# Optimization experiments

Measured on AMD Instinct MI355X. Metric: run time of the kernel, lower is better.

## Reference

```python
import jax, jax.numpy as jnp
import numpy as np

N_NODES = 2048


def setup_inputs() -> dict:
    key = jax.random.key(0)
    ks = jax.random.split(key, 10)
    s = 0.05
    return {
        "x": jax.random.normal(ks[0], (N_NODES, 32), dtype=jnp.float32),
        "centroids": jax.random.normal(ks[1], (N_NODES, 3), dtype=jnp.float32),
        "W_self1": jax.random.normal(ks[2], (35, 64), dtype=jnp.float32) * s,
        "W_neigh1": jax.random.normal(ks[3], (35, 64), dtype=jnp.float32) * s,
        "b1": jnp.zeros((64,), dtype=jnp.float32),
        "W_self2": jax.random.normal(ks[4], (64, 32), dtype=jnp.float32) * s,
        "W_neigh2": jax.random.normal(ks[5], (64, 32), dtype=jnp.float32) * s,
        "b2": jnp.zeros((32,), dtype=jnp.float32),
        "Wm1": jax.random.normal(ks[6], (64, 32), dtype=jnp.float32) * s,
        "bm1": jnp.zeros((32,), dtype=jnp.float32),
        "Wm2": jax.random.normal(ks[7], (32, 2), dtype=jnp.float32) * s,
        "bm2": jnp.zeros((2,), dtype=jnp.float32),
    }


def reference(x, centroids, W_self1, W_neigh1, b1, W_self2, W_neigh2, b2,
              Wm1, bm1, Wm2, bm2):
    n = x.shape[0]
    # Complete DAG edge list: edges i -> j for all i < j (static indices).
    src, dst = jnp.triu_indices(n, k=1)  # each [E], E = n(n-1)/2

    # --- edge features: per-feature cosine-sim vector + |centroid diff| ---
    norms = jnp.linalg.norm(x, axis=1)                       # [N]
    cos = (x[src] * x[dst]) / (norms[src] * norms[dst])[:, None]   # [E,32]
    cdiff = jnp.abs(centroids[src] - centroids[dst])               # [E,3]
    edge_weight = jnp.concatenate([cos, cdiff], axis=1)            # [E,35]

    h = jnp.concatenate([x, centroids], axis=1)                    # [N,35]

    # in-degree of each destination node (mean aggregator denominator)
    deg = jnp.zeros((n,), dtype=h.dtype).at[dst].add(1.0)
    inv_deg = jnp.where(deg > 0, 1.0 / jnp.maximum(deg, 1.0), 0.0)[:, None]

    # --- SAGEConv 1 (mean, with per-feature edge weights) ---
    msg1 = h[src] * edge_weight                                    # [E,35]
    neigh1 = jax.ops.segment_sum(msg1, dst, num_segments=n) * inv_deg
    h1 = h @ W_self1 + neigh1 @ W_neigh1 + b1                      # [N,64]

    # --- SAGEConv 2 (mean, no edge weight) ---
    neigh2 = jax.ops.segment_sum(h1[src], dst, num_segments=n) * inv_deg
    h2 = h1 @ W_self2 + neigh2 @ W_neigh2 + b2                     # [N,32]

    # --- pairwise edge gather + MLP head ---
    ef = jnp.concatenate([h2[src], h2[dst]], axis=1)               # [E,64]
    hid = jax.nn.relu(ef @ Wm1 + bm1)                              # [E,32]
    out = jax.nn.softmax(hid @ Wm2 + bm2, axis=-1)                 # [E,2]
    return out
```

## Files before the change

### kernel.cpp

```cpp
#include <hip/hip_runtime.h>
#include <math.h>

#define N_NODES 2048
#define N1S 36

__device__ __forceinline__ float invdeg(int j) { return j > 0 ? 1.0f / (float)j : 0.0f; }

__global__ __launch_bounds__(256) void k_edgefeat(const float* __restrict__ x,
                                                  const float* __restrict__ cent,
                                                  float* __restrict__ n1) {
  const int tid = threadIdx.x;
  const int bx = blockIdx.x;
  if (bx < 32) {
    __shared__ float invn_s[N_NODES];
    __shared__ float sc[256];
    const int f = bx;
    for (int r = 0; r < 8; ++r) {
      int n = tid + 256 * r;
      const float4* xp = (const float4*)(x + n * 32);
      float s = 0.f;
#pragma unroll
      for (int q = 0; q < 8; ++q) {
        float4 v = xp[q];
        s += v.x * v.x + v.y * v.y + v.z * v.z + v.w * v.w;
      }
      invn_s[n] = rsqrtf(s);
    }
    __syncthreads();
    float sv[8], xv[8];
    float ts = 0.f;
#pragma unroll
    for (int r = 0; r < 8; ++r) {
      int i = tid * 8 + r;
      float xf = x[i * 32 + f];
      xv[r] = xf;
      float s = xf * xf * invn_s[i];
      sv[r] = s;
      ts += s;
    }
    sc[tid] = ts;
    __syncthreads();
    for (int off = 1; off < 256; off <<= 1) {
      float v = (tid >= off) ? sc[tid - off] : 0.f;
      __syncthreads();
      sc[tid] += v;
      __syncthreads();
    }
    float P = sc[tid] - ts;
#pragma unroll
    for (int r = 0; r < 8; ++r) {
      int i = tid * 8 + r;
      n1[i * N1S + f] = P * xv[r] * invn_s[i] * invdeg(i);
      P += sv[r];
    }
  } else {
    __shared__ float cs[N_NODES * 3];
    const float4* cp = (const float4*)cent;
    float4* csp = (float4*)cs;
#pragma unroll
    for (int q = 0; q < 6; ++q) csp[tid + 256 * q] = cp[tid + 256 * q];
    __syncthreads();
    const int w = (bx - 32) * 4 + (tid >> 6);
    const int lane = tid & 63;
#pragma unroll
    for (int pick = 0; pick < 2; ++pick) {
      const int j = pick ? (2047 - w) : w;
      const float cj0 = cs[j * 3 + 0], cj1 = cs[j * 3 + 1], cj2 = cs[j * 3 + 2];
      float s0 = 0.f, s1 = 0.f, s2 = 0.f;
      for (int i = lane; i < j; i += 64) {
        float c0 = cs[i * 3 + 0], c1 = cs[i * 3 + 1], c2 = cs[i * 3 + 2];
        s0 += c0 * fabsf(c0 - cj0);
        s1 += c1 * fabsf(c1 - cj1);
        s2 += c2 * fabsf(c2 - cj2);
      }
#pragma unroll
      for (int d = 32; d > 0; d >>= 1) {
        s0 += __shfl_down(s0, d);
        s1 += __shfl_down(s1, d);
        s2 += __shfl_down(s2, d);
      }
      if (lane == 0) {
        float idg = invdeg(j);
        n1[j * N1S + 32] = s0 * idg;
        n1[j * N1S + 33] = s1 * idg;
        n1[j * N1S + 34] = s2 * idg;
      }
    }
  }
}

__global__ __launch_bounds__(256) void k_h1(const float* __restrict__ x,
                                            const float* __restrict__ cent,
                                            const float* __restrict__ n1,
                                            const float* __restrict__ Ws1,
                                            const float* __restrict__ Wn1,
                                            const float* __restrict__ b1,
                                            float* __restrict__ h1,
                                            float* __restrict__ h1T) {
  const int tid = threadIdx.x;
  const int n = __builtin_amdgcn_readfirstlane(blockIdx.x * 4 + (tid >> 6));
  const int o = tid & 63;
  float acc = b1[o];
  const float4* xr = (const float4*)(x + n * 32);
  const float4* nr = (const float4*)(n1 + n * N1S);
#pragma unroll
  for (int q = 0; q < 8; ++q) {
    float4 xv = xr[q];
    float4 nv = nr[q];
    acc += xv.x * Ws1[(4 * q + 0) * 64 + o] + nv.x * Wn1[(4 * q + 0) * 64 + o];
    acc += xv.y * Ws1[(4 * q + 1) * 64 + o] + nv.y * Wn1[(4 * q + 1) * 64 + o];
    acc += xv.z * Ws1[(4 * q + 2) * 64 + o] + nv.z * Wn1[(4 * q + 2) * 64 + o];
    acc += xv.w * Ws1[(4 * q + 3) * 64 + o] + nv.w * Wn1[(4 * q + 3) * 64 + o];
  }
  {
    float4 nv = nr[8];
    float c0 = cent[n * 3 + 0], c1 = cent[n * 3 + 1], c2 = cent[n * 3 + 2];
    acc += c0 * Ws1[32 * 64 + o] + nv.x * Wn1[32 * 64 + o];
    acc += c1 * Ws1[33 * 64 + o] + nv.y * Wn1[33 * 64 + o];
    acc += c2 * Ws1[34 * 64 + o] + nv.z * Wn1[34 * 64 + o];
  }
  h1[n * 64 + o] = acc;
  h1T[o * N_NODES + n] = acc;
}

__global__ __launch_bounds__(256) void k_scan_h1(const float* __restrict__ h1T,
                                                 float* __restrict__ n2) {
  __shared__ float sc[256];
  const int tid = threadIdx.x;
  const int o = blockIdx.x;
  float sv[8];
  const float4* colp = (const float4*)(h1T + o * N_NODES);
  float4 a = colp[2 * tid];
  float4 b = colp[2 * tid + 1];
  sv[0] = a.x; sv[1] = a.y; sv[2] = a.z; sv[3] = a.w;
  sv[4] = b.x; sv[5] = b.y; sv[6] = b.z; sv[7] = b.w;
  float ts = 0.f;
#pragma unroll
  for (int r = 0; r < 8; ++r) ts += sv[r];
  sc[tid] = ts;
  __syncthreads();
  for (int off = 1; off < 256; off <<= 1) {
    float v = (tid >= off) ? sc[tid - off] : 0.f;
    __syncthreads();
    sc[tid] += v;
    __syncthreads();
  }
  float P = sc[tid] - ts;
#pragma unroll
  for (int r = 0; r < 8; ++r) {
    int i = tid * 8 + r;
    n2[i * 64 + o] = P * invdeg(i);
    P += sv[r];
  }
}

__global__ __launch_bounds__(256) void k_h2AB(const float* __restrict__ h1,
                                              const float* __restrict__ n2,
                                              const float* __restrict__ Ws2,
                                              const float* __restrict__ Wn2,
                                              const float* __restrict__ b2,
                                              const float* __restrict__ Wm1,
                                              const float* __restrict__ bm1,
                                              float* __restrict__ A,
                                              float* __restrict__ Bm) {
  __shared__ float h2s[4][32];
  const int tid = threadIdx.x;
  const int wv = tid >> 6;
  const int lane = tid & 63;
  const int o = lane & 31;
  const int half = lane >> 5;
  const int n = __builtin_amdgcn_readfirstlane(blockIdx.x * 4 + wv);
  float acc = b2[o];
#pragma unroll
  for (int f = 0; f < 64; ++f)
    acc += h1[n * 64 + f] * Ws2[f * 32 + o] + n2[n * 64 + f] * Wn2[f * 32 + o];
  h2s[wv][o] = acc;
  __syncthreads();
  float r = half ? bm1[o] : 0.f;
#pragma unroll
  for (int f = 0; f < 32; ++f)
    r += h2s[wv][f] * Wm1[(half * 32 + f) * 32 + o];
  if (half)
    Bm[n * 32 + o] = r;
  else
    A[n * 32 + o] = r;
}

__global__ __launch_bounds__(256) void k_edges(const float* __restrict__ A,
                                               const float* __restrict__ Bm,
                                               const float* __restrict__ Wm2,
                                               const float* __restrict__ bm2,
                                               float2* __restrict__ out) {
  const int tid = threadIdx.x;
  const int j0 = blockIdx.x * 256;
  const int i0 = blockIdx.y * 8;
  if (i0 >= j0 + 255) return;
  const int j = j0 + tid;
  float Br[32];
  const float4* bp = (const float4*)(Bm + j * 32);
#pragma unroll
  for (int q = 0; q < 8; ++q) {
    float4 v = bp[q];
    Br[4 * q + 0] = v.x;
    Br[4 * q + 1] = v.y;
    Br[4 * q + 2] = v.z;
    Br[4 * q + 3] = v.w;
  }
  float wd[32];
#pragma unroll
  for (int f = 0; f < 32; ++f)
    wd[f] = Wm2[f * 2 + 1] - Wm2[f * 2];
  const float db = bm2[1] - bm2[0];
#pragma unroll
  for (int ii = 0; ii < 8; ++ii) {
    const int i = i0 + ii;
    const float* Ar = A + i * 32;
    float d = db;
#pragma unroll
    for (int f = 0; f < 32; ++f)
      d += fmaxf(Ar[f] + Br[f], 0.f) * wd[f];
    if (i < j) {
      float p0 = 1.0f / (1.0f + __expf(d));
      int e = i * (2 * N_NODES - 1 - i) / 2 + (j - i - 1);
      out[e] = make_float2(p0, 1.0f - p0);
    }
  }
}

extern "C" void kernel_launch(void* const* d_in, const int* in_sizes, int n_in,
                              void* d_out, int out_size, void* d_ws, size_t ws_size,
                              hipStream_t stream) {
  const float* x    = (const float*)d_in[0];
  const float* cent = (const float*)d_in[1];
  const float* Ws1  = (const float*)d_in[2];
  const float* Wn1  = (const float*)d_in[3];
  const float* b1   = (const float*)d_in[4];
  const float* Ws2  = (const float*)d_in[5];
  const float* Wn2  = (const float*)d_in[6];
  const float* b2   = (const float*)d_in[7];
  const float* Wm1  = (const float*)d_in[8];
  const float* bm1  = (const float*)d_in[9];
  const float* Wm2  = (const float*)d_in[10];
  const float* bm2  = (const float*)d_in[11];

  float* ws  = (float*)d_ws;
  float* n1  = ws;
  float* h1  = n1 + 2048 * N1S;
  float* h1T = h1 + 2048 * 64;
  float* n2  = h1T + 2048 * 64;
  float* A   = n2 + 2048 * 64;
  float* Bm  = A + 2048 * 32;

  k_edgefeat<<<288, 256, 0, stream>>>(x, cent, n1);
  k_h1<<<512, 256, 0, stream>>>(x, cent, n1, Ws1, Wn1, b1, h1, h1T);
  k_scan_h1<<<64, 256, 0, stream>>>(h1T, n2);
  k_h2AB<<<512, 256, 0, stream>>>(h1, n2, Ws2, Wn2, b2, Wm1, bm1, A, Bm);
  k_edges<<<dim3(8, 256), 256, 0, stream>>>(A, Bm, Wm2, bm2, (float2*)d_out);
}
```

Measured before the change: 120.8 us.

## Fuse all five stages into one cooperative kernel with grid syncs

```diff
diff --git a/kernel.cpp b/kernel.cpp
--- a/kernel.cpp
+++ b/kernel.cpp
@@ -1,19 +1,33 @@
 #include <hip/hip_runtime.h>
+#include <hip/hip_cooperative_groups.h>
 #include <math.h>
+
+namespace cg = cooperative_groups;
 
 #define N_NODES 2048
 #define N1S 36
+#define NBLK 512
 
 __device__ __forceinline__ float invdeg(int j) { return j > 0 ? 1.0f / (float)j : 0.0f; }
 
-__global__ __launch_bounds__(256) void k_edgefeat(const float* __restrict__ x,
-                                                  const float* __restrict__ cent,
-                                                  float* __restrict__ n1) {
+__global__ __launch_bounds__(256, 2) void k_fused(
+    const float* __restrict__ x, const float* __restrict__ cent,
+    const float* __restrict__ Ws1, const float* __restrict__ Wn1,
+    const float* __restrict__ b1, const float* __restrict__ Ws2,
+    const float* __restrict__ Wn2, const float* __restrict__ b2,
+    const float* __restrict__ Wm1, const float* __restrict__ bm1,
+    const float* __restrict__ Wm2, const float* __restrict__ bm2,
+    float* __restrict__ n1, float* __restrict__ h1, float* __restrict__ h1T,
+    float* __restrict__ n2, float* __restrict__ A, float* __restrict__ Bm,
+    float2* __restrict__ out) {
+  cg::grid_group grid = cg::this_grid();
+  __shared__ float smem[6144];
   const int tid = threadIdx.x;
   const int bx = blockIdx.x;
+
   if (bx < 32) {
-    __shared__ float invn_s[N_NODES];
-    __shared__ float sc[256];
+    float* invn_s = smem;
+    float* sc = smem + 2048;
     const int f = bx;
     for (int r = 0; r < 8; ++r) {
       int n = tid + 256 * r;
@@ -53,8 +67,8 @@
       n1[i * N1S + f] = P * xv[r] * invn_s[i] * invdeg(i);
       P += sv[r];
     }
-  } else {
-    __shared__ float cs[N_NODES * 3];
+  } else if (bx < 288) {
+    float* cs = smem;
     const float4* cp = (const float4*)cent;
     float4* csp = (float4*)cs;
 #pragma unroll
@@ -87,142 +101,127 @@
       }
     }
   }
-}
-
-__global__ __launch_bounds__(256) void k_h1(const float* __restrict__ x,
-                                            const float* __restrict__ cent,
-                                            const float* __restrict__ n1,
-                                            const float* __restrict__ Ws1,
-                                            const float* __restrict__ Wn1,
-                                            const float* __restrict__ b1,
-                                            float* __restrict__ h1,
-                                            float* __restrict__ h1T) {
-  const int tid = threadIdx.x;
-  const int n = __builtin_amdgcn_readfirstlane(blockIdx.x * 4 + (tid >> 6));
-  const int o = tid & 63;
-  float acc = b1[o];
-  const float4* xr = (const float4*)(x + n * 32);
-  const float4* nr = (const float4*)(n1 + n * N1S);
-#pragma unroll
-  for (int q = 0; q < 8; ++q) {
-    float4 xv = xr[q];
-    float4 nv = nr[q];
-    acc += xv.x * Ws1[(4 * q + 0) * 64 + o] + nv.x * Wn1[(4 * q + 0) * 64 + o];
-    acc += xv.y * Ws1[(4 * q + 1) * 64 + o] + nv.y * Wn1[(4 * q + 1) * 64 + o];
-    acc += xv.z * Ws1[(4 * q + 2) * 64 + o] + nv.z * Wn1[(4 * q + 2) * 64 + o];
-    acc += xv.w * Ws1[(4 * q + 3) * 64 + o] + nv.w * Wn1[(4 * q + 3) * 64 + o];
-  }
+  grid.sync();
+
   {
-    float4 nv = nr[8];
-    float c0 = cent[n * 3 + 0], c1 = cent[n * 3 + 1], c2 = cent[n * 3 + 2];
-    acc += c0 * Ws1[32 * 64 + o] + nv.x * Wn1[32 * 64 + o];
-    acc += c1 * Ws1[33 * 64 + o] + nv.y * Wn1[33 * 64 + o];
-    acc += c2 * Ws1[34 * 64 + o] + nv.z * Wn1[34 * 64 + o];
-  }
-  h1[n * 64 + o] = acc;
-  h1T[o * N_NODES + n] = acc;
-}
-
-__global__ __launch_bounds__(256) void k_scan_h1(const float* __restrict__ h1T,
-                                                 float* __restrict__ n2) {
-  __shared__ float sc[256];
-  const int tid = threadIdx.x;
-  const int o = blockIdx.x;
-  float sv[8];
-  const float4* colp = (const float4*)(h1T + o * N_NODES);
-  float4 a = colp[2 * tid];
-  float4 b = colp[2 * tid + 1];
-  sv[0] = a.x; sv[1] = a.y; sv[2] = a.z; sv[3] = a.w;
-  sv[4] = b.x; sv[5] = b.y; sv[6] = b.z; sv[7] = b.w;
-  float ts = 0.f;
-#pragma unroll
-  for (int r = 0; r < 8; ++r) ts += sv[r];
-  sc[tid] = ts;
-  __syncthreads();
-  for (int off = 1; off < 256; off <<= 1) {
-    float v = (tid >= off) ? sc[tid - off] : 0.f;
-    __syncthreads();
-    sc[tid] += v;
-    __syncthreads();
-  }
-  float P = sc[tid] - ts;
-#pragma unroll
-  for (int r = 0; r < 8; ++r) {
-    int i = tid * 8 + r;
-    n2[i * 64 + o] = P * invdeg(i);
-    P += sv[r];
-  }
-}
-
-__global__ __launch_bounds__(256) void k_h2AB(const float* __restrict__ h1,
-                                              const float* __restrict__ n2,
-                                              const float* __restrict__ Ws2,
-                                              const float* __restrict__ Wn2,
-                                              const float* __restrict__ b2,
-                                              const float* __restrict__ Wm1,
-                                              const float* __restrict__ bm1,
-                                              float* __restrict__ A,
-                                              float* __restrict__ Bm) {
-  __shared__ float h2s[4][32];
-  const int tid = threadIdx.x;
-  const int wv = tid >> 6;
-  const int lane = tid & 63;
-  const int o = lane & 31;
-  const int half = lane >> 5;
-  const int n = __builtin_amdgcn_readfirstlane(blockIdx.x * 4 + wv);
-  float acc = b2[o];
-#pragma unroll
-  for (int f = 0; f < 64; ++f)
-    acc += h1[n * 64 + f] * Ws2[f * 32 + o] + n2[n * 64 + f] * Wn2[f * 32 + o];
-  h2s[wv][o] = acc;
-  __syncthreads();
-  float r = half ? bm1[o] : 0.f;
-#pragma unroll
-  for (int f = 0; f < 32; ++f)
-    r += h2s[wv][f] * Wm1[(half * 32 + f) * 32 + o];
-  if (half)
-    Bm[n * 32 + o] = r;
-  else
-    A[n * 32 + o] = r;
-}
-
-__global__ __launch_bounds__(256) void k_edges(const float* __restrict__ A,
-                                               const float* __restrict__ Bm,
-                                               const float* __restrict__ Wm2,
-                                               const float* __restrict__ bm2,
-                                               float2* __restrict__ out) {
-  const int tid = threadIdx.x;
-  const int j0 = blockIdx.x * 256;
-  const int i0 = blockIdx.y * 8;
-  if (i0 >= j0 + 255) return;
-  const int j = j0 + tid;
-  float Br[32];
-  const float4* bp = (const float4*)(Bm + j * 32);
-#pragma unroll
-  for (int q = 0; q < 8; ++q) {
-    float4 v = bp[q];
-    Br[4 * q + 0] = v.x;
-    Br[4 * q + 1] = v.y;
-    Br[4 * q + 2] = v.z;
-    Br[4 * q + 3] = v.w;
-  }
-  float wd[32];
-#pragma unroll
-  for (int f = 0; f < 32; ++f)
-    wd[f] = Wm2[f * 2 + 1] - Wm2[f * 2];
-  const float db = bm2[1] - bm2[0];
-#pragma unroll
-  for (int ii = 0; ii < 8; ++ii) {
-    const int i = i0 + ii;
-    const float* Ar = A + i * 32;
-    float d = db;
+    const int n = __builtin_amdgcn_readfirstlane(bx * 4 + (tid >> 6));
+    const int o = tid & 63;
+    float acc = b1[o];
+    const float4* xr = (const float4*)(x + n * 32);
+    const float4* nr = (const float4*)(n1 + n * N1S);
+#pragma unroll
+    for (int q = 0; q < 8; ++q) {
+      float4 xv = xr[q];
+      float4 nv = nr[q];
+      acc += xv.x * Ws1[(4 * q + 0) * 64 + o] + nv.x * Wn1[(4 * q + 0) * 64 + o];
+      acc += xv.y * Ws1[(4 * q + 1) * 64 + o] + nv.y * Wn1[(4 * q + 1) * 64 + o];
+      acc += xv.z * Ws1[(4 * q + 2) * 64 + o] + nv.z * Wn1[(4 * q + 2) * 64 + o];
+      acc += xv.w * Ws1[(4 * q + 3) * 64 + o] + nv.w * Wn1[(4 * q + 3) * 64 + o];
+    }
+    {
+      float4 nv = nr[8];
+      float c0 = cent[n * 3 + 0], c1 = cent[n * 3 + 1], c2 = cent[n * 3 + 2];
+      acc += c0 * Ws1[32 * 64 + o] + nv.x * Wn1[32 * 64 + o];
+      acc += c1 * Ws1[33 * 64 + o] + nv.y * Wn1[33 * 64 + o];
+      acc += c2 * Ws1[34 * 64 + o] + nv.z * Wn1[34 * 64 + o];
+    }
+    h1[n * 64 + o] = acc;
+    h1T[o * N_NODES + n] = acc;
+  }
+  grid.sync();
+
+  if (bx < 64) {
+    float* sc = smem;
+    const int o = bx;
+    float sv[8];
+    const float4* colp = (const float4*)(h1T + o * N_NODES);
+    float4 a = colp[2 * tid];
+    float4 b = colp[2 * tid + 1];
+    sv[0] = a.x; sv[1] = a.y; sv[2] = a.z; sv[3] = a.w;
+    sv[4] = b.x; sv[5] = b.y; sv[6] = b.z; sv[7] = b.w;
+    float ts = 0.f;
+#pragma unroll
+    for (int r = 0; r < 8; ++r) ts += sv[r];
+    sc[tid] = ts;
+    __syncthreads();
+    for (int off = 1; off < 256; off <<= 1) {
+      float v = (tid >= off) ? sc[tid - off] : 0.f;
+      __syncthreads();
+      sc[tid] += v;
+      __syncthreads();
+    }
+    float P = sc[tid] - ts;
+#pragma unroll
+    for (int r = 0; r < 8; ++r) {
+      int i = tid * 8 + r;
+      n2[i * 64 + o] = P * invdeg(i);
+      P += sv[r];
+    }
+  }
+  grid.sync();
+
+  {
+    float* h2s = smem;
+    const int wv = tid >> 6;
+    const int lane = tid & 63;
+    const int o = lane & 31;
+    const int half = lane >> 5;
+    const int n = __builtin_amdgcn_readfirstlane(bx * 4 + wv);
+    float acc = b2[o];
+#pragma unroll
+    for (int f = 0; f < 64; ++f)
+      acc += h1[n * 64 + f] * Ws2[f * 32 + o] + n2[n * 64 + f] * Wn2[f * 32 + o];
+    h2s[wv * 32 + o] = acc;
+    __syncthreads();
+    float r = half ? bm1[o] : 0.f;
 #pragma unroll
     for (int f = 0; f < 32; ++f)
-      d += fmaxf(Ar[f] + Br[f], 0.f) * wd[f];
-    if (i < j) {
-      float p0 = 1.0f / (1.0f + __expf(d));
-      int e = i * (2 * N_NODES - 1 - i) / 2 + (j - i - 1);
-      out[e] = make_float2(p0, 1.0f - p0);
+      r += h2s[wv * 32 + f] * Wm1[(half * 32 + f) * 32 + o];
+    if (half)
+      Bm[n * 32 + o] = r;
+    else
+      A[n * 32 + o] = r;
+  }
+  grid.sync();
+
+  {
+    float wd[32];
+#pragma unroll
+    for (int f = 0; f < 32; ++f)
+      wd[f] = Wm2[f * 2 + 1] - Wm2[f * 2];
+    const float db = bm2[1] - bm2[0];
+    for (int s = bx; s < 1152; s += NBLK) {
+      int bxe = 0;
+#pragma unroll
+      for (int k = 1; k < 8; ++k) bxe += (s >= 16 * k * (k + 1)) ? 1 : 0;
+      const int bye = s - 16 * bxe * (bxe + 1);
+      const int j0 = bxe * 256;
+      const int i0 = bye * 8;
+      const int j = j0 + tid;
+      float Br[32];
+      const float4* bp = (const float4*)(Bm + j * 32);
+#pragma unroll
+      for (int q = 0; q < 8; ++q) {
+        float4 v = bp[q];
+        Br[4 * q + 0] = v.x;
+        Br[4 * q + 1] = v.y;
+        Br[4 * q + 2] = v.z;
+        Br[4 * q + 3] = v.w;
+      }
+#pragma unroll
+      for (int ii = 0; ii < 8; ++ii) {
+        const int i = i0 + ii;
+        const float* Ar = A + i * 32;
+        float d = db;
+#pragma unroll
+        for (int f = 0; f < 32; ++f)
+          d += fmaxf(Ar[f] + Br[f], 0.f) * wd[f];
+        if (i < j) {
+          float p0 = 1.0f / (1.0f + __expf(d));
+          int e = i * (2 * N_NODES - 1 - i) / 2 + (j - i - 1);
+          out[e] = make_float2(p0, 1.0f - p0);
+        }
+      }
     }
   }
 }
@@ -250,10 +249,10 @@
   float* n2  = h1T + 2048 * 64;
   float* A   = n2 + 2048 * 64;
   float* Bm  = A + 2048 * 32;
-
-  k_edgefeat<<<288, 256, 0, stream>>>(x, cent, n1);
-  k_h1<<<512, 256, 0, stream>>>(x, cent, n1, Ws1, Wn1, b1, h1, h1T);
-  k_scan_h1<<<64, 256, 0, stream>>>(h1T, n2);
-  k_h2AB<<<512, 256, 0, stream>>>(h1, n2, Ws2, Wn2, b2, Wm1, bm1, A, Bm);
-  k_edges<<<dim3(8, 256), 256, 0, stream>>>(A, Bm, Wm2, bm2, (float2*)d_out);
+  float2* outp = (float2*)d_out;
+
+  void* args[] = {&x, &cent, &Ws1, &Wn1, &b1, &Ws2, &Wn2, &b2,
+                  &Wm1, &bm1, &Wm2, &bm2,
+                  &n1, &h1, &h1T, &n2, &A, &Bm, &outp};
+  hipLaunchCooperativeKernel((void*)k_fused, dim3(NBLK), dim3(256), args, 0, stream);
 }
```

Measured after the change: 342.4 us. 183% more time.

## Fuse h1 prefix-sum scan into neighbouring kernels and compact triangular edge grid

Applied to the files above, without the earlier changes.

```diff
diff --git a/kernel.cpp b/kernel.cpp
--- a/kernel.cpp
+++ b/kernel.cpp
@@ -96,9 +96,11 @@
                                             const float* __restrict__ Wn1,
                                             const float* __restrict__ b1,
                                             float* __restrict__ h1,
-                                            float* __restrict__ h1T) {
-  const int tid = threadIdx.x;
-  const int n = __builtin_amdgcn_readfirstlane(blockIdx.x * 4 + (tid >> 6));
+                                            float* __restrict__ csum) {
+  __shared__ float h1s[4][64];
+  const int tid = threadIdx.x;
+  const int wv = tid >> 6;
+  const int n = __builtin_amdgcn_readfirstlane(blockIdx.x * 4 + wv);
   const int o = tid & 63;
   float acc = b1[o];
   const float4* xr = (const float4*)(x + n * 32);
@@ -120,42 +122,15 @@
     acc += c2 * Ws1[34 * 64 + o] + nv.z * Wn1[34 * 64 + o];
   }
   h1[n * 64 + o] = acc;
-  h1T[o * N_NODES + n] = acc;
-}
-
-__global__ __launch_bounds__(256) void k_scan_h1(const float* __restrict__ h1T,
-                                                 float* __restrict__ n2) {
-  __shared__ float sc[256];
-  const int tid = threadIdx.x;
-  const int o = blockIdx.x;
-  float sv[8];
-  const float4* colp = (const float4*)(h1T + o * N_NODES);
-  float4 a = colp[2 * tid];
-  float4 b = colp[2 * tid + 1];
-  sv[0] = a.x; sv[1] = a.y; sv[2] = a.z; sv[3] = a.w;
-  sv[4] = b.x; sv[5] = b.y; sv[6] = b.z; sv[7] = b.w;
-  float ts = 0.f;
-#pragma unroll
-  for (int r = 0; r < 8; ++r) ts += sv[r];
-  sc[tid] = ts;
-  __syncthreads();
-  for (int off = 1; off < 256; off <<= 1) {
-    float v = (tid >= off) ? sc[tid - off] : 0.f;
-    __syncthreads();
-    sc[tid] += v;
-    __syncthreads();
-  }
-  float P = sc[tid] - ts;
-#pragma unroll
-  for (int r = 0; r < 8; ++r) {
-    int i = tid * 8 + r;
-    n2[i * 64 + o] = P * invdeg(i);
-    P += sv[r];
-  }
+  h1s[wv][o] = acc;
+  __syncthreads();
+  if (tid < 64)
+    csum[blockIdx.x * 64 + tid] =
+        h1s[0][tid] + h1s[1][tid] + h1s[2][tid] + h1s[3][tid];
 }
 
 __global__ __launch_bounds__(256) void k_h2AB(const float* __restrict__ h1,
-                                              const float* __restrict__ n2,
+                                              const float* __restrict__ csum,
                                               const float* __restrict__ Ws2,
                                               const float* __restrict__ Wn2,
                                               const float* __restrict__ b2,
@@ -163,27 +138,40 @@
                                               const float* __restrict__ bm1,
                                               float* __restrict__ A,
                                               float* __restrict__ Bm) {
-  __shared__ float h2s[4][32];
+  __shared__ float part[4][64], h1s[4][64], n2s[4][64], h2s[4][32];
   const int tid = threadIdx.x;
   const int wv = tid >> 6;
   const int lane = tid & 63;
-  const int o = lane & 31;
-  const int half = lane >> 5;
-  const int n = __builtin_amdgcn_readfirstlane(blockIdx.x * 4 + wv);
-  float acc = b2[o];
+  const int c = blockIdx.x;
+  const int o = lane;
+  float p = 0.f;
+  for (int cc = wv; cc < c; cc += 4) p += csum[cc * 64 + o];
+  part[wv][o] = p;
+  const int n = __builtin_amdgcn_readfirstlane(c * 4 + wv);
+  const float hv = h1[n * 64 + o];
+  h1s[wv][o] = hv;
+  __syncthreads();
+  float S = part[0][o] + part[1][o] + part[2][o] + part[3][o];
+#pragma unroll
+  for (int k = 0; k < 3; ++k)
+    if (k < wv) S += h1s[k][o];
+  n2s[wv][o] = S * invdeg(n);
+  __syncthreads();
+  const int oo = lane & 31, half = lane >> 5;
+  float acc = b2[oo];
 #pragma unroll
   for (int f = 0; f < 64; ++f)
-    acc += h1[n * 64 + f] * Ws2[f * 32 + o] + n2[n * 64 + f] * Wn2[f * 32 + o];
-  h2s[wv][o] = acc;
-  __syncthreads();
-  float r = half ? bm1[o] : 0.f;
+    acc += h1s[wv][f] * Ws2[f * 32 + oo] + n2s[wv][f] * Wn2[f * 32 + oo];
+  h2s[wv][oo] = acc;
+  __syncthreads();
+  float r = half ? bm1[oo] : 0.f;
 #pragma unroll
   for (int f = 0; f < 32; ++f)
-    r += h2s[wv][f] * Wm1[(half * 32 + f) * 32 + o];
+    r += h2s[wv][f] * Wm1[(half * 32 + f) * 32 + oo];
   if (half)
-    Bm[n * 32 + o] = r;
+    Bm[n * 32 + oo] = r;
   else
-    A[n * 32 + o] = r;
+    A[n * 32 + oo] = r;
 }
 
 __global__ __launch_bounds__(256) void k_edges(const float* __restrict__ A,
@@ -192,9 +180,13 @@
                                                const float* __restrict__ bm2,
                                                float2* __restrict__ out) {
   const int tid = threadIdx.x;
-  const int j0 = blockIdx.x * 256;
-  const int i0 = blockIdx.y * 8;
-  if (i0 >= j0 + 255) return;
+  const int s = blockIdx.x;
+  int bxe = 0;
+#pragma unroll
+  for (int k = 1; k < 8; ++k) bxe += (s >= 16 * k * (k + 1)) ? 1 : 0;
+  const int bye = s - 16 * bxe * (bxe + 1);
+  const int j0 = bxe * 256;
+  const int i0 = bye * 8;
   const int j = j0 + tid;
   float Br[32];
   const float4* bp = (const float4*)(Bm + j * 32);
@@ -243,17 +235,15 @@
   const float* Wm2  = (const float*)d_in[10];
   const float* bm2  = (const float*)d_in[11];
 
-  float* ws  = (float*)d_ws;
-  float* n1  = ws;
-  float* h1  = n1 + 2048 * N1S;
-  float* h1T = h1 + 2048 * 64;
-  float* n2  = h1T + 2048 * 64;
-  float* A   = n2 + 2048 * 64;
-  float* Bm  = A + 2048 * 32;
+  float* ws   = (float*)d_ws;
+  float* n1   = ws;
+  float* h1   = n1 + 2048 * N1S;
+  float* csum = h1 + 2048 * 64;
+  float* A    = csum + 512 * 64;
+  float* Bm   = A + 2048 * 32;
 
   k_edgefeat<<<288, 256, 0, stream>>>(x, cent, n1);
-  k_h1<<<512, 256, 0, stream>>>(x, cent, n1, Ws1, Wn1, b1, h1, h1T);
-  k_scan_h1<<<64, 256, 0, stream>>>(h1T, n2);
-  k_h2AB<<<512, 256, 0, stream>>>(h1, n2, Ws2, Wn2, b2, Wm1, bm1, A, Bm);
-  k_edges<<<dim3(8, 256), 256, 0, stream>>>(A, Bm, Wm2, bm2, (float2*)d_out);
-}
+  k_h1<<<512, 256, 0, stream>>>(x, cent, n1, Ws1, Wn1, b1, h1, csum);
+  k_h2AB<<<512, 256, 0, stream>>>(h1, csum, Ws2, Wn2, b2, Wm1, bm1, A, Bm);
+  k_edges<<<1152, 256, 0, stream>>>(A, Bm, Wm2, bm2, (float2*)d_out);
+}
```

After: 141.9 us, median of 2. 17.5% more time.
